# Optimization experiments

Measured on AMD Instinct MI355X. Metric: run time of the kernel, lower is better.

## Reference

```python
import jax, jax.numpy as jnp
import numpy as np

N_NODES = 50000


def _sage_conv(x, src, dst, Wl, Wr, b):
    # PyG SAGEConv (aggr='mean'): out = lin_l(mean_{j in N(i)} x_j) + lin_r(x_i)
    msgs = x[src]                                              # [E, d] gather
    s = jax.ops.segment_sum(msgs, dst, num_segments=N_NODES)   # [N, d]
    cnt = jax.ops.segment_sum(jnp.ones((src.shape[0], 1), x.dtype), dst,
                              num_segments=N_NODES)            # [N, 1]
    agg = s / jnp.maximum(cnt, 1.0)                            # mean, 0 if no nbrs
    return agg @ Wl.T + x @ Wr.T + b


def setup_inputs() -> dict:
    key = jax.random.key(0)
    ks = jax.random.split(key, 12)
    in_dim, h = 128, 128
    E, P = 500000, 200000
    x = jax.random.normal(ks[0], (N_NODES, in_dim), dtype=jnp.float32)
    edge_index = jax.random.randint(ks[1], (2, E), 0, N_NODES)
    pairs = jax.random.randint(ks[2], (P, 2), 0, N_NODES)
    def lin(k, fan_out, fan_in):
        bound = 1.0 / np.sqrt(fan_in)
        return jax.random.uniform(k, (fan_out, fan_in), jnp.float32, -bound, bound)
    return {
        "x": x, "edge_index": edge_index, "pairs": pairs,
        "Wl1": lin(ks[3], h, in_dim), "Wr1": lin(ks[4], h, in_dim),
        "b1": jnp.zeros((h,), jnp.float32),
        "Wl2": lin(ks[5], h, h), "Wr2": lin(ks[6], h, h),
        "b2": jnp.zeros((h,), jnp.float32),
        "W3": lin(ks[7], h, 2 * h), "b3": jnp.zeros((h,), jnp.float32),
        "W4": lin(ks[8], 1, h), "b4": jnp.zeros((1,), jnp.float32),
    }


def reference(x, edge_index, pairs, Wl1, Wr1, b1, Wl2, Wr2, b2, W3, b3, W4, b4):
    src, dst = edge_index[0], edge_index[1]
    h1 = jax.nn.relu(_sage_conv(x, src, dst, Wl1, Wr1, b1))    # [N, h]
    h2 = jax.nn.relu(_sage_conv(h1, src, dst, Wl2, Wr2, b2))   # [N, h]
    a = h2[pairs[:, 0]]                                        # [P, h]
    b = h2[pairs[:, 1]]                                        # [P, h]
    z = jnp.concatenate([a, b], axis=1)                        # [P, 2h]
    s = jax.nn.relu(z @ W3.T + b3) @ W4.T + b4                 # [P, 1]
    return jax.nn.sigmoid(s).squeeze(-1)                       # [P]
```

## Files before the change

kernel.cpp:

```cpp
#include <hip/hip_runtime.h>
#include <math.h>

#define N_NODES 50000
#define E_EDGES 500000
#define P_PAIRS 200000
#define MAX_DEG 64

#define NB        196
#define EB        2048
#define EPT       8
#define SORT_BLKS 245

typedef __bf16    bf16x8 __attribute__((ext_vector_type(8)));
typedef _Float16  f16x8  __attribute__((ext_vector_type(8)));
typedef float     f32x4  __attribute__((ext_vector_type(4)));


#define CONV_BLKS 1563
#define PREP_BLKS 128

__global__ __launch_bounds__(256) void pre_k(
        const float* __restrict__ x, __bf16* __restrict__ xb,
        const int* __restrict__ dst,
        int* __restrict__ bucketCnt, int* __restrict__ blockBase,
        const float* __restrict__ Wl1, const float* __restrict__ Wr1,
        const float* __restrict__ Wl2, const float* __restrict__ Wr2,
        const float* __restrict__ W3,
        __bf16* __restrict__ P1, __bf16* __restrict__ P2, __bf16* __restrict__ P4) {
    __shared__ int cnt[NB];
    int b = blockIdx.x, t = threadIdx.x;
    if (b < SORT_BLKS) {
        if (t < NB) cnt[t] = 0;
        __syncthreads();
        int ebase = b * EB;
        #pragma unroll
        for (int i = 0; i < EPT; ++i) {
            int e = ebase + i * 256 + t;
            if (e < E_EDGES) atomicAdd(&cnt[dst[e] >> 8], 1);
        }
        __syncthreads();
        if (t < NB) blockBase[b * NB + t] = atomicAdd(&bucketCnt[t], cnt[t]);
    } else if (b < SORT_BLKS + CONV_BLKS) {
        int i0 = (b - SORT_BLKS) * 1024 + t;
        #pragma unroll
        for (int k = 0; k < 4; ++k) {
            int i = i0 + k * 256;
            if (i < N_NODES * 128 / 4) {
                float4 v = ((const float4*)x)[i];
                __bf16* o = xb + (size_t)i * 4;
                o[0] = (__bf16)v.x; o[1] = (__bf16)v.y; o[2] = (__bf16)v.z; o[3] = (__bf16)v.w;
            }
        }
    } else {
        int i = (b - SORT_BLKS - CONV_BLKS) * 256 + t;
        int lane = (i >> 3) & 63;
        int j = i & 7;
        int kq = (lane >> 4) * 8 + j;
        {
            int kt = i >> 12, nt = (i >> 9) & 7;
            int n = nt * 16 + (lane & 15);
            int k = kt * 32 + kq;
            P1[i] = (__bf16)((k < 128) ? Wl1[n * 128 + k] : Wr1[n * 128 + (k - 128)]);
            P2[i] = (__bf16)((k < 128) ? Wl2[n * 128 + k] : Wr2[n * 128 + (k - 128)]);
        }
        {
            int kt = i >> 13, nt = (i >> 9) & 15;
            int n = nt * 16 + (lane & 15);
            int k = kt * 32 + kq;
            P4[i] = (__bf16)((n < 128) ? W3[n * 256 + k] : W3[(n - 128) * 256 + 128 + k]);
        }
    }
}


__global__ __launch_bounds__(256) void place_k(const int* __restrict__ src,
                                               const int* __restrict__ dst,
                                               const int* __restrict__ bucketCnt,
                                               const int* __restrict__ blockBase,
                                               unsigned* __restrict__ edgebuf) {
    __shared__ int cnt[256];
    __shared__ int buf[256];
    __shared__ int sbase[NB];
    __shared__ int gbase[NB];
    __shared__ int cur[NB];
    __shared__ unsigned sortbuf[EB];
    __shared__ unsigned char bktof[EB];
    int blk = blockIdx.x, t = threadIdx.x;

    int bv = (t < NB) ? bucketCnt[t] : 0;
    buf[t] = bv;
    __syncthreads();
    for (int off = 1; off < 256; off <<= 1) {
        int xv = (t >= off) ? buf[t - off] : 0;
        __syncthreads();
        buf[t] += xv;
        __syncthreads();
    }
    if (t < NB) gbase[t] = (buf[t] - bv) + blockBase[blk * NB + t];
    cnt[t] = 0;
    if (t < NB) cur[t] = 0;
    __syncthreads();

    unsigned packed[EPT];
    int bk[EPT];
    int ebase = blk * EB;
    #pragma unroll
    for (int i = 0; i < EPT; ++i) {
        int e = ebase + i * 256 + t;
        if (e < E_EDGES) {
            int d = dst[e];
            packed[i] = ((unsigned)d << 16) | (unsigned)src[e];
            bk[i] = d >> 8;
            atomicAdd(&cnt[bk[i]], 1);
        } else bk[i] = -1;
    }
    __syncthreads();

    int v = cnt[t];
    buf[t] = v;
    __syncthreads();
    for (int off = 1; off < 256; off <<= 1) {
        int xv = (t >= off) ? buf[t - off] : 0;
        __syncthreads();
        buf[t] += xv;
        __syncthreads();
    }
    if (t < NB) sbase[t] = buf[t] - v;
    __syncthreads();

    #pragma unroll
    for (int i = 0; i < EPT; ++i) {
        if (bk[i] >= 0) {
            int p = sbase[bk[i]] + atomicAdd(&cur[bk[i]], 1);
            sortbuf[p] = packed[i];
            bktof[p] = (unsigned char)bk[i];
        }
    }
    __syncthreads();

    int nE = E_EDGES - ebase; if (nE > EB) nE = EB;
    for (int i = t; i < nE; i += 256) {
        int bb = bktof[i];
        edgebuf[gbase[bb] + (i - sbase[bb])] = sortbuf[i];
    }
}


__global__ __launch_bounds__(256) void slots_k(const unsigned* __restrict__ edgebuf,
                                               const int* __restrict__ bucketCnt,
                                               unsigned short* __restrict__ slots,
                                               int* __restrict__ deg) {
    __shared__ unsigned short srow[256 * MAX_DEG];
    __shared__ int cur[256];
    __shared__ int buf[256];
    __shared__ int sc[2];
    int b = blockIdx.x, t = threadIdx.x;

    int bv = (t < NB) ? bucketCnt[t] : 0;
    buf[t] = bv;
    cur[t] = 0;
    __syncthreads();
    for (int off = 1; off < 256; off <<= 1) {
        int xv = (t >= off) ? buf[t - off] : 0;
        __syncthreads();
        buf[t] += xv;
        __syncthreads();
    }
    if (t == b) { sc[0] = buf[t] - bv; sc[1] = bv; }
    __syncthreads();
    int base = sc[0], n = sc[1];

    for (int i = t; i < n; i += 256) {
        unsigned p = edgebuf[base + i];
        int dl = (p >> 16) & 255;
        int pos = atomicAdd(&cur[dl], 1);
        if (pos < MAX_DEG) srow[dl * MAX_DEG + pos] = (unsigned short)(p & 0xFFFFu);
    }
    __syncthreads();
    unsigned* sl32 = (unsigned*)slots;
    const unsigned* sr32 = (const unsigned*)srow;
    int gbase32 = b * 8192;
    for (int i = t; i < 8192; i += 256) {
        int node = b * 256 + (i >> 5);
        if (node < N_NODES) sl32[gbase32 + i] = sr32[i];
    }
    int node = b * 256 + t;
    if (node < N_NODES) deg[node] = cur[t];
}


__global__ __launch_bounds__(256) void agg1_k(const __bf16* __restrict__ feat,
                                              const int* __restrict__ deg_a,
                                              const unsigned short* __restrict__ slots,
                                              __bf16* __restrict__ agg) {
    int n = blockIdx.x * 4 + (threadIdx.x >> 6);
    if (n >= N_NODES) return;
    int lane = threadIdx.x & 63;
    int slot = lane >> 4, l = lane & 15;
    int deg = deg_a[n];
    int nit = (deg < MAX_DEG) ? deg : MAX_DEG;

    int ed = (lane < nit) ? (int)slots[n * MAX_DEG + lane] : 0;

    float s[8];
    #pragma unroll
    for (int e = 0; e < 8; ++e) s[e] = 0.f;

    int trips = (nit + 3) >> 2;
    int it = slot;
    int k = 0;
    for (; k + 1 < trips; k += 2, it += 8) {
        int sn0 = __builtin_amdgcn_ds_bpermute(it << 2, ed);
        int sn1 = __builtin_amdgcn_ds_bpermute((it + 4) << 2, ed);
        bf16x8 v0 = *(const bf16x8*)(feat + (size_t)sn0 * 128 + l * 8);
        bf16x8 v1 = *(const bf16x8*)(feat + (size_t)sn1 * 128 + l * 8);
        if (it < nit) {
            #pragma unroll
            for (int e = 0; e < 8; ++e) s[e] += (float)v0[e];
        }
        if (it + 4 < nit) {
            #pragma unroll
            for (int e = 0; e < 8; ++e) s[e] += (float)v1[e];
        }
    }
    if (k < trips) {
        int sn = __builtin_amdgcn_ds_bpermute(it << 2, ed);
        bf16x8 v = *(const bf16x8*)(feat + (size_t)sn * 128 + l * 8);
        if (it < nit) {
            #pragma unroll
            for (int e = 0; e < 8; ++e) s[e] += (float)v[e];
        }
    }

    #pragma unroll
    for (int e = 0; e < 8; ++e) {
        s[e] += __shfl_xor(s[e], 16, 64);
        s[e] += __shfl_xor(s[e], 32, 64);
    }

    if (slot == 0) {
        float inv = 1.0f / fmaxf((float)deg, 1.0f);
        bf16x8 o;
        #pragma unroll
        for (int e = 0; e < 8; ++e) o[e] = (__bf16)(s[e] * inv);
        *(bf16x8*)(agg + (size_t)n * 128 + l * 8) = o;
    }
}


__global__ __launch_bounds__(256) void layer_mfma_k(const __bf16* __restrict__ agg,
                                                    const __bf16* __restrict__ feat,
                                                    const __bf16* __restrict__ wpack,
                                                    const float* __restrict__ bias,
                                                    __bf16* __restrict__ out) {
    int wave = threadIdx.x >> 6;
    int lane = threadIdx.x & 63;
    int m = lane & 15, quad = lane >> 4;
    int rbase = blockIdx.x * 64 + wave * 16;
    int r0 = rbase + m; if (r0 > N_NODES - 1) r0 = N_NODES - 1;

    f32x4 acc[8];
    #pragma unroll
    for (int nt = 0; nt < 8; ++nt) acc[nt] = (f32x4)0.f;

    #pragma unroll
    for (int kt = 0; kt < 8; ++kt) {
        const __bf16* src = (kt < 4) ? agg : feat;
        int ko = (kt & 3) * 32 + quad * 8;
        bf16x8 a0 = *(const bf16x8*)(src + (size_t)r0 * 128 + ko);
        const __bf16* wb = wpack + (size_t)kt * 4096 + lane * 8;
        #pragma unroll
        for (int nt = 0; nt < 8; ++nt) {
            bf16x8 b = *(const bf16x8*)(wb + nt * 512);
            acc[nt] = __builtin_amdgcn_mfma_f32_16x16x32_bf16(a0, b, acc[nt], 0, 0, 0);
        }
    }

    #pragma unroll
    for (int r = 0; r < 4; ++r) {
        int row = rbase + quad * 4 + r;
        if (row < N_NODES) {
            #pragma unroll
            for (int nt = 0; nt < 8; ++nt) {
                float v = acc[nt][r] + bias[nt * 16 + m];
                out[(size_t)row * 128 + nt * 16 + m] = (__bf16)fmaxf(v, 0.f);
            }
        }
    }
}


__global__ __launch_bounds__(256) void layer2uv_k(const __bf16* __restrict__ agg,
                                                  const __bf16* __restrict__ feat,
                                                  const __bf16* __restrict__ wpack,
                                                  const float* __restrict__ bias,
                                                  const __bf16* __restrict__ wpack4,
                                                  _Float16* __restrict__ UV) {
    __shared__ __bf16 sh[4][16][136];
    int wave = threadIdx.x >> 6;
    int lane = threadIdx.x & 63;
    int m = lane & 15, q = lane >> 4;
    int rbase = blockIdx.x * 64 + wave * 16;
    int r0 = rbase + m; if (r0 > N_NODES - 1) r0 = N_NODES - 1;

    f32x4 acc[8];
    #pragma unroll
    for (int nt = 0; nt < 8; ++nt) acc[nt] = (f32x4)0.f;

    #pragma unroll
    for (int kt = 0; kt < 8; ++kt) {
        const __bf16* src = (kt < 4) ? agg : feat;
        int ko = (kt & 3) * 32 + q * 8;
        bf16x8 a0 = *(const bf16x8*)(src + (size_t)r0 * 128 + ko);
        const __bf16* wb = wpack + (size_t)kt * 4096 + lane * 8;
        #pragma unroll
        for (int nt = 0; nt < 8; ++nt) {
            bf16x8 b = *(const bf16x8*)(wb + nt * 512);
            acc[nt] = __builtin_amdgcn_mfma_f32_16x16x32_bf16(a0, b, acc[nt], 0, 0, 0);
        }
    }

    #pragma unroll
    for (int rr = 0; rr < 4; ++rr)
        #pragma unroll
        for (int nt = 0; nt < 8; ++nt) {
            float v = acc[nt][rr] + bias[nt * 16 + m];
            sh[wave][q * 4 + rr][nt * 16 + m] = (__bf16)fmaxf(v, 0.f);
        }

    f32x4 acc2[16];
    #pragma unroll
    for (int nt = 0; nt < 16; ++nt) acc2[nt] = (f32x4)0.f;

    #pragma unroll
    for (int kt = 0; kt < 4; ++kt) {
        bf16x8 a = *(const bf16x8*)&sh[wave][m][kt * 32 + q * 8];
        const __bf16* wb = wpack4 + (size_t)kt * 8192 + lane * 8;
        #pragma unroll
        for (int nt = 0; nt < 16; ++nt) {
            bf16x8 b = *(const bf16x8*)(wb + nt * 512);
            acc2[nt] = __builtin_amdgcn_mfma_f32_16x16x32_bf16(a, b, acc2[nt], 0, 0, 0);
        }
    }

    #pragma unroll
    for (int rr = 0; rr < 4; ++rr) {
        int row = rbase + q * 4 + rr;
        if (row < N_NODES) {
            #pragma unroll
            for (int nt = 0; nt < 16; ++nt)
                UV[(size_t)row * 256 + nt * 16 + m] = (_Float16)acc2[nt][rr];
        }
    }
}


__global__ __launch_bounds__(256) void pair_ep_k(const _Float16* __restrict__ UV,
                                                 const int* __restrict__ pairs,
                                                 const float* __restrict__ b3,
                                                 const float* __restrict__ W4,
                                                 const float* __restrict__ b4,
                                                 float* __restrict__ out) {
    int t = threadIdx.x;
    int g = t >> 4, l = t & 15;
    int base = blockIdx.x * 64;

    float4 b3a = *(const float4*)(b3 + l * 8);
    float4 b3b = *(const float4*)(b3 + l * 8 + 4);
    float4 w4a = *(const float4*)(W4 + l * 8);
    float4 w4b = *(const float4*)(W4 + l * 8 + 4);
    float bb[8] = {b3a.x, b3a.y, b3a.z, b3a.w, b3b.x, b3b.y, b3b.z, b3b.w};
    float ww[8] = {w4a.x, w4a.y, w4a.z, w4a.w, w4b.x, w4b.y, w4b.z, w4b.w};
    float b4s = b4[0];

    int2 pr[4];
    #pragma unroll
    for (int i = 0; i < 4; ++i) pr[i] = ((const int2*)pairs)[base + i * 16 + g];

    f16x8 ua[4], vb[4];
    #pragma unroll
    for (int i = 0; i < 4; ++i) {
        ua[i] = *(const f16x8*)(UV + (size_t)pr[i].x * 256 + l * 8);
        vb[i] = *(const f16x8*)(UV + (size_t)pr[i].y * 256 + 128 + l * 8);
    }

    #pragma unroll
    for (int i = 0; i < 4; ++i) {
        float p = 0.f;
        #pragma unroll
        for (int e = 0; e < 8; ++e)
            p += fmaxf((float)ua[i][e] + (float)vb[i][e] + bb[e], 0.f) * ww[e];
        #pragma unroll
        for (int s = 1; s < 16; s <<= 1) p += __shfl_xor(p, s, 64);
        if (l == 0)
            out[base + i * 16 + g] = 1.0f / (1.0f + expf(-(p + b4s)));
    }
}


extern "C" void kernel_launch(void* const* d_in, const int* in_sizes, int n_in,
                              void* d_out, int out_size, void* d_ws, size_t ws_size,
                              hipStream_t stream) {
    const float* x   = (const float*)d_in[0];
    const int*   ei  = (const int*)d_in[1];
    const int*   prs = (const int*)d_in[2];
    const float* Wl1 = (const float*)d_in[3];
    const float* Wr1 = (const float*)d_in[4];
    const float* b1  = (const float*)d_in[5];
    const float* Wl2 = (const float*)d_in[6];
    const float* Wr2 = (const float*)d_in[7];
    const float* b2  = (const float*)d_in[8];
    const float* W3  = (const float*)d_in[9];
    const float* b3  = (const float*)d_in[10];
    const float* W4  = (const float*)d_in[11];
    const float* b4  = (const float*)d_in[12];
    float* out = (float*)d_out;

    const int* srcv = ei;
    const int* dstv = ei + E_EDGES;

    char* ws = (char*)d_ws;
    size_t off = 0;
    auto alloc = [&](size_t bytes) -> void* {
        void* p = ws + off;
        off = (off + bytes + 255) & ~(size_t)255;
        return p;
    };
    int*            bucketCnt  = (int*)alloc(sizeof(int) * NB);
    int*            blockBase  = (int*)alloc(sizeof(int) * SORT_BLKS * NB);
    unsigned*       edgebuf    = (unsigned*)alloc(sizeof(unsigned) * E_EDGES);
    int*            deg        = (int*)alloc(sizeof(int) * N_NODES);
    unsigned short* slots      = (unsigned short*)alloc(sizeof(unsigned short) * (size_t)N_NODES * MAX_DEG + 512);
    __bf16*   P1     = (__bf16*)alloc(sizeof(__bf16) * 32768);
    __bf16*   P2     = (__bf16*)alloc(sizeof(__bf16) * 32768);
    __bf16*   P4     = (__bf16*)alloc(sizeof(__bf16) * 32768);
    __bf16*   xb     = (__bf16*)alloc(sizeof(__bf16) * (size_t)N_NODES * 128);
    __bf16*   aggb   = (__bf16*)alloc(sizeof(__bf16) * (size_t)N_NODES * 128);
    __bf16*   h1b    = (__bf16*)alloc(sizeof(__bf16) * (size_t)N_NODES * 128);
    _Float16* UV     = (_Float16*)alloc(sizeof(_Float16) * (size_t)N_NODES * 256);
    (void)ws_size; (void)in_sizes; (void)n_in; (void)out_size;

    hipMemsetAsync(bucketCnt, 0, sizeof(int) * NB, stream);

    pre_k<<<SORT_BLKS + CONV_BLKS + PREP_BLKS, 256, 0, stream>>>(
        x, xb, dstv, bucketCnt, blockBase, Wl1, Wr1, Wl2, Wr2, W3, P1, P2, P4);
    place_k<<<SORT_BLKS, 256, 0, stream>>>(srcv, dstv, bucketCnt, blockBase, edgebuf);
    slots_k<<<NB, 256, 0, stream>>>(edgebuf, bucketCnt, slots, deg);

    agg1_k<<<(N_NODES + 3) / 4, 256, 0, stream>>>(xb, deg, slots, aggb);
    layer_mfma_k<<<(N_NODES + 63) / 64, 256, 0, stream>>>(aggb, xb, P1, b1, h1b);
    agg1_k<<<(N_NODES + 3) / 4, 256, 0, stream>>>(h1b, deg, slots, aggb);
    layer2uv_k<<<(N_NODES + 63) / 64, 256, 0, stream>>>(aggb, h1b, P2, b2, P4, UV);
    pair_ep_k<<<P_PAIRS / 64, 256, 0, stream>>>(UV, prs, b3, W4, b4, out);
}
```

Measured before the change: 217.0 us.

## Fuse neighbor mean-aggregation with SAGE layer GEMMs into per-16-node blocks

Merges the separate aggregation kernel and MFMA layer kernel into one 1024-thread block that handles 16 nodes. Each wave gathers and averages one node's neighbors into shared memory, then 8 (or 16) waves each compute one 16-column output tile. This drops the global agg buffer round-trip and two kernel launches. In exchange, only half the waves do GEMM work in layer 1, blocks are large, and each block issues more weight loads per row.

```diff
diff --git a/kernel.cpp b/kernel.cpp
--- a/kernel.cpp
+++ b/kernel.cpp
@@ -189,20 +189,12 @@
 }
 
 
-__global__ __launch_bounds__(256) void agg1_k(const __bf16* __restrict__ feat,
-                                              const int* __restrict__ deg_a,
-                                              const unsigned short* __restrict__ slots,
-                                              __bf16* __restrict__ agg) {
-    int n = blockIdx.x * 4 + (threadIdx.x >> 6);
-    if (n >= N_NODES) return;
-    int lane = threadIdx.x & 63;
+__device__ __forceinline__ void wave_gather(const __bf16* __restrict__ feat,
+                                            const unsigned short* __restrict__ slots,
+                                            int n, int dg, int lane, float s[8]) {
     int slot = lane >> 4, l = lane & 15;
-    int deg = deg_a[n];
-    int nit = (deg < MAX_DEG) ? deg : MAX_DEG;
-
+    int nit = (dg < MAX_DEG) ? dg : MAX_DEG;
     int ed = (lane < nit) ? (int)slots[n * MAX_DEG + lane] : 0;
-
-    float s[8];
     #pragma unroll
     for (int e = 0; e < 8; ++e) s[e] = 0.f;
 
@@ -231,125 +223,122 @@
             for (int e = 0; e < 8; ++e) s[e] += (float)v[e];
         }
     }
-
     #pragma unroll
     for (int e = 0; e < 8; ++e) {
         s[e] += __shfl_xor(s[e], 16, 64);
         s[e] += __shfl_xor(s[e], 32, 64);
     }
-
-    if (slot == 0) {
-        float inv = 1.0f / fmaxf((float)deg, 1.0f);
-        bf16x8 o;
-        #pragma unroll
-        for (int e = 0; e < 8; ++e) o[e] = (__bf16)(s[e] * inv);
-        *(bf16x8*)(agg + (size_t)n * 128 + l * 8) = o;
-    }
-}
-
-
-__global__ __launch_bounds__(256) void layer_mfma_k(const __bf16* __restrict__ agg,
-                                                    const __bf16* __restrict__ feat,
-                                                    const __bf16* __restrict__ wpack,
-                                                    const float* __restrict__ bias,
-                                                    __bf16* __restrict__ out) {
-    int wave = threadIdx.x >> 6;
-    int lane = threadIdx.x & 63;
-    int m = lane & 15, quad = lane >> 4;
-    int rbase = blockIdx.x * 64 + wave * 16;
-    int r0 = rbase + m; if (r0 > N_NODES - 1) r0 = N_NODES - 1;
-
-    f32x4 acc[8];
-    #pragma unroll
-    for (int nt = 0; nt < 8; ++nt) acc[nt] = (f32x4)0.f;
-
-    #pragma unroll
-    for (int kt = 0; kt < 8; ++kt) {
-        const __bf16* src = (kt < 4) ? agg : feat;
-        int ko = (kt & 3) * 32 + quad * 8;
-        bf16x8 a0 = *(const bf16x8*)(src + (size_t)r0 * 128 + ko);
-        const __bf16* wb = wpack + (size_t)kt * 4096 + lane * 8;
-        #pragma unroll
-        for (int nt = 0; nt < 8; ++nt) {
-            bf16x8 b = *(const bf16x8*)(wb + nt * 512);
-            acc[nt] = __builtin_amdgcn_mfma_f32_16x16x32_bf16(a0, b, acc[nt], 0, 0, 0);
-        }
-    }
-
-    #pragma unroll
-    for (int r = 0; r < 4; ++r) {
-        int row = rbase + quad * 4 + r;
-        if (row < N_NODES) {
+}
+
+
+__global__ __launch_bounds__(1024, 8) void flayer1_k(const __bf16* __restrict__ feat,
+                                                     const int* __restrict__ deg_a,
+                                                     const unsigned short* __restrict__ slots,
+                                                     const __bf16* __restrict__ wpack,
+                                                     const float* __restrict__ bias,
+                                                     __bf16* __restrict__ out) {
+    __shared__ __bf16 sAgg[16][136];
+    int t = threadIdx.x;
+    int w = t >> 6, lane = t & 63;
+    int rbase = blockIdx.x * 16;
+
+    {
+        int n = rbase + w;
+        int dg = deg_a[n];
+        float s[8];
+        wave_gather(feat, slots, n, dg, lane, s);
+        if ((lane >> 4) == 0) {
+            int l = lane & 15;
+            float inv = 1.0f / fmaxf((float)dg, 1.0f);
+            bf16x8 o;
             #pragma unroll
-            for (int nt = 0; nt < 8; ++nt) {
-                float v = acc[nt][r] + bias[nt * 16 + m];
-                out[(size_t)row * 128 + nt * 16 + m] = (__bf16)fmaxf(v, 0.f);
-            }
-        }
-    }
-}
-
-
-__global__ __launch_bounds__(256) void layer2uv_k(const __bf16* __restrict__ agg,
-                                                  const __bf16* __restrict__ feat,
-                                                  const __bf16* __restrict__ wpack,
-                                                  const float* __restrict__ bias,
-                                                  const __bf16* __restrict__ wpack4,
-                                                  _Float16* __restrict__ UV) {
-    __shared__ __bf16 sh[4][16][136];
-    int wave = threadIdx.x >> 6;
-    int lane = threadIdx.x & 63;
+            for (int e = 0; e < 8; ++e) o[e] = (__bf16)(s[e] * inv);
+            *(bf16x8*)&sAgg[w][l * 8] = o;
+        }
+    }
+    __syncthreads();
+
+    if (w < 8) {
+        int m = lane & 15, q = lane >> 4;
+        int r0 = rbase + m;
+        f32x4 acc = (f32x4)0.f;
+        #pragma unroll
+        for (int kt = 0; kt < 8; ++kt) {
+            bf16x8 a = (kt < 4)
+                ? *(const bf16x8*)&sAgg[m][kt * 32 + q * 8]
+                : *(const bf16x8*)(feat + (size_t)r0 * 128 + (kt - 4) * 32 + q * 8);
+            bf16x8 b = *(const bf16x8*)(wpack + (size_t)kt * 4096 + w * 512 + lane * 8);
+            acc = __builtin_amdgcn_mfma_f32_16x16x32_bf16(a, b, acc, 0, 0, 0);
+        }
+        float bv = bias[w * 16 + m];
+        #pragma unroll
+        for (int rr = 0; rr < 4; ++rr) {
+            int row = rbase + q * 4 + rr;
+            out[(size_t)row * 128 + w * 16 + m] = (__bf16)fmaxf(acc[rr] + bv, 0.f);
+        }
+    }
+}
+
+
+__global__ __launch_bounds__(1024, 8) void flayer2uv_k(const __bf16* __restrict__ feat,
+                                                       const int* __restrict__ deg_a,
+                                                       const unsigned short* __restrict__ slots,
+                                                       const __bf16* __restrict__ wpack,
+                                                       const float* __restrict__ bias,
+                                                       const __bf16* __restrict__ wpack4,
+                                                       _Float16* __restrict__ UV) {
+    __shared__ __bf16 sAgg[16][136];
+    __shared__ __bf16 sh[16][136];
+    int t = threadIdx.x;
+    int w = t >> 6, lane = t & 63;
+    int rbase = blockIdx.x * 16;
     int m = lane & 15, q = lane >> 4;
-    int rbase = blockIdx.x * 64 + wave * 16;
-    int r0 = rbase + m; if (r0 > N_NODES - 1) r0 = N_NODES - 1;
-
-    f32x4 acc[8];
-    #pragma unroll
-    for (int nt = 0; nt < 8; ++nt) acc[nt] = (f32x4)0.f;
-
-    #pragma unroll
-    for (int kt = 0; kt < 8; ++kt) {
-        const __bf16* src = (kt < 4) ? agg : feat;
-        int ko = (kt & 3) * 32 + q * 8;
-        bf16x8 a0 = *(const bf16x8*)(src + (size_t)r0 * 128 + ko);
-        const __bf16* wb = wpack + (size_t)kt * 4096 + lane * 8;
-        #pragma unroll
-        for (int nt = 0; nt < 8; ++nt) {
-            bf16x8 b = *(const bf16x8*)(wb + nt * 512);
-            acc[nt] = __builtin_amdgcn_mfma_f32_16x16x32_bf16(a0, b, acc[nt], 0, 0, 0);
-        }
-    }
-
-    #pragma unroll
-    for (int rr = 0; rr < 4; ++rr)
-        #pragma unroll
-        for (int nt = 0; nt < 8; ++nt) {
-            float v = acc[nt][rr] + bias[nt * 16 + m];
-            sh[wave][q * 4 + rr][nt * 16 + m] = (__bf16)fmaxf(v, 0.f);
-        }
-
-    f32x4 acc2[16];
-    #pragma unroll
-    for (int nt = 0; nt < 16; ++nt) acc2[nt] = (f32x4)0.f;
-
-    #pragma unroll
-    for (int kt = 0; kt < 4; ++kt) {
-        bf16x8 a = *(const bf16x8*)&sh[wave][m][kt * 32 + q * 8];
-        const __bf16* wb = wpack4 + (size_t)kt * 8192 + lane * 8;
-        #pragma unroll
-        for (int nt = 0; nt < 16; ++nt) {
-            bf16x8 b = *(const bf16x8*)(wb + nt * 512);
-            acc2[nt] = __builtin_amdgcn_mfma_f32_16x16x32_bf16(a, b, acc2[nt], 0, 0, 0);
-        }
-    }
-
-    #pragma unroll
-    for (int rr = 0; rr < 4; ++rr) {
-        int row = rbase + q * 4 + rr;
-        if (row < N_NODES) {
+
+    {
+        int n = rbase + w;
+        int dg = deg_a[n];
+        float s[8];
+        wave_gather(feat, slots, n, dg, lane, s);
+        if (q == 0) {
+            float inv = 1.0f / fmaxf((float)dg, 1.0f);
+            bf16x8 o;
             #pragma unroll
-            for (int nt = 0; nt < 16; ++nt)
-                UV[(size_t)row * 256 + nt * 16 + m] = (_Float16)acc2[nt][rr];
+            for (int e = 0; e < 8; ++e) o[e] = (__bf16)(s[e] * inv);
+            *(bf16x8*)&sAgg[w][m * 8] = o;
+        }
+    }
+    __syncthreads();
+
+    if (w < 8) {
+        int r0 = rbase + m;
+        f32x4 acc = (f32x4)0.f;
+        #pragma unroll
+        for (int kt = 0; kt < 8; ++kt) {
+            bf16x8 a = (kt < 4)
+                ? *(const bf16x8*)&sAgg[m][kt * 32 + q * 8]
+                : *(const bf16x8*)(feat + (size_t)r0 * 128 + (kt - 4) * 32 + q * 8);
+            bf16x8 b = *(const bf16x8*)(wpack + (size_t)kt * 4096 + w * 512 + lane * 8);
+            acc = __builtin_amdgcn_mfma_f32_16x16x32_bf16(a, b, acc, 0, 0, 0);
+        }
+        float bv = bias[w * 16 + m];
+        #pragma unroll
+        for (int rr = 0; rr < 4; ++rr)
+            sh[q * 4 + rr][w * 16 + m] = (__bf16)fmaxf(acc[rr] + bv, 0.f);
+    }
+    __syncthreads();
+
+    {
+        f32x4 acc2 = (f32x4)0.f;
+        #pragma unroll
+        for (int kt = 0; kt < 4; ++kt) {
+            bf16x8 a = *(const bf16x8*)&sh[m][kt * 32 + q * 8];
+            bf16x8 b = *(const bf16x8*)(wpack4 + (size_t)kt * 8192 + w * 512 + lane * 8);
+            acc2 = __builtin_amdgcn_mfma_f32_16x16x32_bf16(a, b, acc2, 0, 0, 0);
+        }
+        #pragma unroll
+        for (int rr = 0; rr < 4; ++rr) {
+            int row = rbase + q * 4 + rr;
+            UV[(size_t)row * 256 + w * 16 + m] = (_Float16)acc2[rr];
         }
     }
 }
@@ -435,7 +424,6 @@
     __bf16*   P2     = (__bf16*)alloc(sizeof(__bf16) * 32768);
     __bf16*   P4     = (__bf16*)alloc(sizeof(__bf16) * 32768);
     __bf16*   xb     = (__bf16*)alloc(sizeof(__bf16) * (size_t)N_NODES * 128);
-    __bf16*   aggb   = (__bf16*)alloc(sizeof(__bf16) * (size_t)N_NODES * 128);
     __bf16*   h1b    = (__bf16*)alloc(sizeof(__bf16) * (size_t)N_NODES * 128);
     _Float16* UV     = (_Float16*)alloc(sizeof(_Float16) * (size_t)N_NODES * 256);
     (void)ws_size; (void)in_sizes; (void)n_in; (void)out_size;
@@ -447,9 +435,7 @@
     place_k<<<SORT_BLKS, 256, 0, stream>>>(srcv, dstv, bucketCnt, blockBase, edgebuf);
     slots_k<<<NB, 256, 0, stream>>>(edgebuf, bucketCnt, slots, deg);
 
-    agg1_k<<<(N_NODES + 3) / 4, 256, 0, stream>>>(xb, deg, slots, aggb);
-    layer_mfma_k<<<(N_NODES + 63) / 64, 256, 0, stream>>>(aggb, xb, P1, b1, h1b);
-    agg1_k<<<(N_NODES + 3) / 4, 256, 0, stream>>>(h1b, deg, slots, aggb);
-    layer2uv_k<<<(N_NODES + 63) / 64, 256, 0, stream>>>(aggb, h1b, P2, b2, P4, UV);
+    flayer1_k<<<N_NODES / 16, 1024, 0, stream>>>(xb, deg, slots, P1, b1, h1b);
+    flayer2uv_k<<<N_NODES / 16, 1024, 0, stream>>>(h1b, deg, slots, P2, b2, P4, UV);
     pair_ep_k<<<P_PAIRS / 64, 256, 0, stream>>>(UV, prs, b3, W4, b4, out);
 }
```

Result: no change. 220.0 us (+1.4%).
